# Kernel optimization log

Measured on AMD Instinct MI355X. Metric: run time of the kernel, lower is better.

The kernel has to match this reference:

```python
import jax, jax.numpy as jnp
import numpy as np
import math

CEN_W = 1.0
ANG_W = 1.0


def _radius(ndim):
    # Iterative version of the recursive Radius() from the source.
    if ndim < 1:
        raise ValueError('ndim >= 1 required')
    if ndim == 1:
        return 0.0
    r = 0.5
    for _ in range(3, ndim + 1):
        r = 0.5 / math.sqrt(1.0 - r * r)
    return r


def _costheta(ndim):
    return 2.0 * _radius(ndim - 1) ** 2 - 1.0


def setup_inputs() -> dict:
    key = jax.random.key(0)
    k1, k2, k3 = jax.random.split(key, 3)
    B, C, D = 65536, 1000, 512
    y = jax.random.randint(k1, (B,), 0, C, dtype=jnp.int64 if jax.config.jax_enable_x64 else jnp.int32)
    feat = jax.random.normal(k2, (B, D), dtype=jnp.float32)
    centers = jax.random.normal(k3, (C, D), dtype=jnp.float32)
    return {"y": y, "feat": feat, "centers": centers}


def reference(y, feat, centers):
    C = centers.shape[0]
    B = feat.shape[0]
    ct = jnp.float32(_costheta(C))  # static Python constant from num_classes

    # ---- center loss: gather assigned centers, squared diff sum ----
    centers_pred = centers[y]                      # [B, D] gather
    diff = feat - centers_pred
    loss_cen = 0.5 * jnp.sum(diff * diff) / B

    # ---- angular loss: vectorized Gram matrix over classes ----
    # In torch, centers[j].data and dist are detached -> stop_gradient here.
    centers_sg = jax.lax.stop_gradient(centers)
    dist = jnp.linalg.norm(centers_sg, axis=1)     # [C], detached
    gram = centers @ centers_sg.T                  # [C, C]; grad flows via rows only
    sim = gram / (dist[:, None] * dist[None, :])
    offdiag = 1.0 - jnp.eye(C, dtype=sim.dtype)
    loss_ang = jnp.sum(offdiag * (sim - ct) ** 2) / (0.5 * C * (C - 1))

    return loss_cen * CEN_W + loss_ang * ANG_W
```

## Files before the change

### kernel.cpp

```cpp
#include <hip/hip_runtime.h>
#include <math.h>

typedef __attribute__((ext_vector_type(8))) short bf16x8;
typedef __attribute__((ext_vector_type(16))) float f32x16;
typedef __attribute__((ext_vector_type(4))) float vf4;
typedef __attribute__((ext_vector_type(4))) unsigned int u32x4;

__device__ __forceinline__ float wave_reduce(float v) {
#pragma unroll
    for (int off = 32; off > 0; off >>= 1) v += __shfl_down(v, off, 64);
    return v;
}

__device__ __forceinline__ unsigned int pk_trunc(float f0, float f1) {
    unsigned u0 = __float_as_uint(f0), u1 = __float_as_uint(f1);
    return (u1 & 0xFFFF0000u) | (u0 >> 16);
}

__global__ __launch_bounds__(256) void fused_kernel(const int* __restrict__ y,
                                                    const vf4* __restrict__ feat4,
                                                    const vf4* __restrict__ cent4,
                                                    float* __restrict__ partials,
                                                    int n4, int d4, float cen_scale,
                                                    int C, int ntile32, int steps16,
                                                    float ct, float ang_scale) {
    const int bid = blockIdx.x;
    const int lane = threadIdx.x & 63;
    const int wid = threadIdx.x >> 6;
    __shared__ float sm[4];

    float partial = 0.f;

    const int t = bid * 4 + wid;
    const int ntile2 = ntile32 * ntile32;
    if (t < ntile2) {
        const int ti = t / ntile32;
        const int tj = t - ti * ntile32;
        const int m = lane & 31;
        const int half = lane >> 5;
        const int ra = ti * 32 + m;
        const int rb = tj * 32 + m;
        const bool va = ra < C;
        const bool vb = rb < C;
        const vf4* aptr = cent4 + (size_t)ra * d4 + half * 2;
        const vf4* bptr = cent4 + (size_t)rb * d4 + half * 2;
        f32x16 acc;
#pragma unroll
        for (int k = 0; k < 16; ++k) acc[k] = 0.f;
        float sa = 0.f, sb = 0.f;
#pragma unroll 4
        for (int st = 0; st < steps16; ++st) {
            vf4 a0 = {0.f, 0.f, 0.f, 0.f}, a1 = a0, b0 = a0, b1 = a0;
            if (va) { a0 = aptr[st * 4]; a1 = aptr[st * 4 + 1]; }
            if (vb) { b0 = bptr[st * 4]; b1 = bptr[st * 4 + 1]; }
            sa += a0.x * a0.x + a0.y * a0.y + a0.z * a0.z + a0.w * a0.w
                + a1.x * a1.x + a1.y * a1.y + a1.z * a1.z + a1.w * a1.w;
            sb += b0.x * b0.x + b0.y * b0.y + b0.z * b0.z + b0.w * b0.w
                + b1.x * b1.x + b1.y * b1.y + b1.z * b1.z + b1.w * b1.w;
            u32x4 ap, bp;
            ap.x = pk_trunc(a0.x, a0.y); ap.y = pk_trunc(a0.z, a0.w);
            ap.z = pk_trunc(a1.x, a1.y); ap.w = pk_trunc(a1.z, a1.w);
            bp.x = pk_trunc(b0.x, b0.y); bp.y = pk_trunc(b0.z, b0.w);
            bp.z = pk_trunc(b1.x, b1.y); bp.w = pk_trunc(b1.z, b1.w);
            bf16x8 af = __builtin_bit_cast(bf16x8, ap);
            bf16x8 bf = __builtin_bit_cast(bf16x8, bp);
            acc = __builtin_amdgcn_mfma_f32_32x32x16_bf16(af, bf, acc, 0, 0, 0);
        }
        sa += __shfl_xor(sa, 32, 64);
        sb += __shfl_xor(sb, 32, 64);
        const int gj = tj * 32 + m;
        const float dj = sb;
        float local = 0.f;
#pragma unroll
        for (int reg = 0; reg < 16; ++reg) {
            const int r = (reg & 3) + 8 * (reg >> 2) + 4 * half;
            const int gi = ti * 32 + r;
            const float di = __shfl(sa, r, 64);
            if (gi < C && gj < C && gi != gj) {
                float sim = acc[reg] * rsqrtf(di * dj);
                float dlt = sim - ct;
                local += dlt * dlt;
            }
        }
        partial = local * ang_scale;
    }

    {
        const int stride = gridDim.x * 256;
        float cs = 0.f;
        int i = bid * 256 + threadIdx.x;
        if ((stride % d4) == 0) {
            if (i < n4) {
                int row = i / d4;
                const int col = i - row * d4;
                const int rstep = stride / d4;
                for (; i < n4; i += stride, row += rstep) {
                    const int cls = y[row];
                    vf4 f = __builtin_nontemporal_load(feat4 + i);
                    vf4 c = cent4[(size_t)cls * d4 + col];
                    float dx = f.x - c.x, dy = f.y - c.y, dz = f.z - c.z, dw = f.w - c.w;
                    cs += dx * dx + dy * dy + dz * dz + dw * dw;
                }
            }
        } else {
            for (; i < n4; i += stride) {
                int row = i / d4;
                int col = i - row * d4;
                const int cls = y[row];
                vf4 f = __builtin_nontemporal_load(feat4 + i);
                vf4 c = cent4[(size_t)cls * d4 + col];
                float dx = f.x - c.x, dy = f.y - c.y, dz = f.z - c.z, dw = f.w - c.w;
                cs += dx * dx + dy * dy + dz * dz + dw * dw;
            }
        }
        partial += cs * cen_scale;
    }

    float r = wave_reduce(partial);
    if (lane == 0) sm[wid] = r;
    __syncthreads();
    if (threadIdx.x == 0) {
        partials[bid] = sm[0] + sm[1] + sm[2] + sm[3];
    }
}

__global__ __launch_bounds__(256) void reduce_kernel(const float* __restrict__ partials,
                                                     float* __restrict__ out, int nb) {
    __shared__ float sm[4];
    const int lane = threadIdx.x & 63;
    const int wid = threadIdx.x >> 6;
    float s = 0.f;
    for (int i = threadIdx.x; i < nb; i += 256) s += partials[i];
    s = wave_reduce(s);
    if (lane == 0) sm[wid] = s;
    __syncthreads();
    if (threadIdx.x == 0) out[0] = sm[0] + sm[1] + sm[2] + sm[3];
}

extern "C" void kernel_launch(void* const* d_in, const int* in_sizes, int n_in,
                              void* d_out, int out_size, void* d_ws, size_t ws_size,
                              hipStream_t stream) {
    const int* y = (const int*)d_in[0];
    const float* feat = (const float*)d_in[1];
    const float* centers = (const float*)d_in[2];

    const int B = in_sizes[0];
    const int D = in_sizes[1] / B;
    const int C = in_sizes[2] / D;
    const int d4 = D / 4;
    const int ntile32 = (C + 31) / 32;

    const int nd = C - 1;
    double r = 0.0;
    if (nd >= 2) {
        r = 0.5;
        for (int i = 3; i <= nd; ++i) r = 0.5 / sqrt(1.0 - r * r);
    }
    const float ct = (float)(2.0 * r * r - 1.0);

    const float cen_scale = (float)(0.5 / (double)B);
    const float ang_scale = (float)(1.0 / (0.5 * (double)C * (double)(C - 1)));

    float* partials = (float*)d_ws;
    const int nb = 8192;

    fused_kernel<<<nb, 256, 0, stream>>>(
        y, (const vf4*)feat, (const vf4*)centers, partials,
        B * d4, d4, cen_scale, C, ntile32, D / 16, ct, ang_scale);

    reduce_kernel<<<1, 256, 0, stream>>>(partials, (float*)d_out, nb);
}
```

Baseline: 210.6 us.

## Exploit Gram symmetry, unroll center-loss loads, fuse final reduction via atomic counter

The angular part now computes only the upper-triangular 32x32 tiles of the Gram matrix and weights off-diagonal tiles by two, roughly halving the MFMA work and center reloads. The center-loss loop is replaced, for the exact-fit shape, by four independent feature and gather loads per thread to expose memory-level parallelism. The separate reduce kernel is dropped in favour of a last-block-done reduction using an atomic counter, which is zeroed with a memset before launch. This saves a kernel launch but adds a memset and relies on the fast-path shape conditions and the threadfence ordering.

Result: slower. 569.0 us (+170.1%).

```diff
diff --git a/kernel.cpp b/kernel.cpp
--- a/kernel.cpp
+++ b/kernel.cpp
@@ -21,21 +21,33 @@
                                                     const vf4* __restrict__ feat4,
                                                     const vf4* __restrict__ cent4,
                                                     float* __restrict__ partials,
+                                                    unsigned int* __restrict__ counter,
+                                                    float* __restrict__ out,
                                                     int n4, int d4, float cen_scale,
-                                                    int C, int ntile32, int steps16,
-                                                    float ct, float ang_scale) {
+                                                    int C, int ntile32, int ntri,
+                                                    int steps16, float ct, float ang_scale) {
     const int bid = blockIdx.x;
     const int lane = threadIdx.x & 63;
     const int wid = threadIdx.x >> 6;
     __shared__ float sm[4];
+    __shared__ bool is_last;
 
     float partial = 0.f;
 
     const int t = bid * 4 + wid;
-    const int ntile2 = ntile32 * ntile32;
-    if (t < ntile2) {
-        const int ti = t / ntile32;
-        const int tj = t - ti * ntile32;
+    if (t < ntri) {
+        const int N = ntile32;
+        const float ff = (float)((2 * N + 1) * (2 * N + 1) - 8 * t);
+        int ti = (int)(((float)(2 * N + 1) - sqrtf(ff)) * 0.5f);
+        int base = ti * N - (ti * (ti - 1)) / 2;
+        if (t < base) {
+            --ti; base = ti * N - (ti * (ti - 1)) / 2;
+        } else {
+            const int nxt = (ti + 1) * N - ((ti + 1) * ti) / 2;
+            if (t >= nxt) { ++ti; base = nxt; }
+        }
+        const int tj = ti + (t - base);
+
         const int m = lane & 31;
         const int half = lane >> 5;
         const int ra = ti * 32 + m;
@@ -82,26 +94,41 @@
                 local += dlt * dlt;
             }
         }
-        partial = local * ang_scale;
+        const float w = (ti == tj) ? 1.f : 2.f;
+        partial = local * (ang_scale * w);
     }
 
     {
         const int stride = gridDim.x * 256;
         float cs = 0.f;
         int i = bid * 256 + threadIdx.x;
-        if ((stride % d4) == 0) {
-            if (i < n4) {
-                int row = i / d4;
-                const int col = i - row * d4;
-                const int rstep = stride / d4;
-                for (; i < n4; i += stride, row += rstep) {
-                    const int cls = y[row];
-                    vf4 f = __builtin_nontemporal_load(feat4 + i);
-                    vf4 c = cent4[(size_t)cls * d4 + col];
-                    float dx = f.x - c.x, dy = f.y - c.y, dz = f.z - c.z, dw = f.w - c.w;
-                    cs += dx * dx + dy * dy + dz * dz + dw * dw;
-                }
-            }
+        const bool fast = ((stride % d4) == 0) && ((d4 & 63) == 0) && (n4 == 4 * stride);
+        if (fast) {
+            int row = i / d4;
+            const int col = i - row * d4;
+            const int rstep = stride / d4;
+            const vf4 f0 = __builtin_nontemporal_load(feat4 + i);
+            const vf4 f1 = __builtin_nontemporal_load(feat4 + i + stride);
+            const vf4 f2 = __builtin_nontemporal_load(feat4 + i + 2 * stride);
+            const vf4 f3 = __builtin_nontemporal_load(feat4 + i + 3 * stride);
+            const int r0 = __builtin_amdgcn_readfirstlane(row);
+            const int cls0 = y[r0];
+            const int cls1 = y[r0 + rstep];
+            const int cls2 = y[r0 + 2 * rstep];
+            const int cls3 = y[r0 + 3 * rstep];
+            const vf4 g0 = cent4[(size_t)cls0 * d4 + col];
+            const vf4 g1 = cent4[(size_t)cls1 * d4 + col];
+            const vf4 g2 = cent4[(size_t)cls2 * d4 + col];
+            const vf4 g3 = cent4[(size_t)cls3 * d4 + col];
+            float dx, dy, dz, dw;
+            dx = f0.x - g0.x; dy = f0.y - g0.y; dz = f0.z - g0.z; dw = f0.w - g0.w;
+            cs += dx * dx + dy * dy + dz * dz + dw * dw;
+            dx = f1.x - g1.x; dy = f1.y - g1.y; dz = f1.z - g1.z; dw = f1.w - g1.w;
+            cs += dx * dx + dy * dy + dz * dz + dw * dw;
+            dx = f2.x - g2.x; dy = f2.y - g2.y; dz = f2.z - g2.z; dw = f2.w - g2.w;
+            cs += dx * dx + dy * dy + dz * dz + dw * dw;
+            dx = f3.x - g3.x; dy = f3.y - g3.y; dz = f3.z - g3.z; dw = f3.w - g3.w;
+            cs += dx * dx + dy * dy + dz * dz + dw * dw;
         } else {
             for (; i < n4; i += stride) {
                 int row = i / d4;
@@ -121,20 +148,21 @@
     __syncthreads();
     if (threadIdx.x == 0) {
         partials[bid] = sm[0] + sm[1] + sm[2] + sm[3];
-    }
-}
-
-__global__ __launch_bounds__(256) void reduce_kernel(const float* __restrict__ partials,
-                                                     float* __restrict__ out, int nb) {
-    __shared__ float sm[4];
-    const int lane = threadIdx.x & 63;
-    const int wid = threadIdx.x >> 6;
-    float s = 0.f;
-    for (int i = threadIdx.x; i < nb; i += 256) s += partials[i];
-    s = wave_reduce(s);
-    if (lane == 0) sm[wid] = s;
+        __threadfence();
+        const unsigned int old = atomicAdd(counter, 1u);
+        is_last = (old == gridDim.x - 1);
+    }
     __syncthreads();
-    if (threadIdx.x == 0) out[0] = sm[0] + sm[1] + sm[2] + sm[3];
+    if (is_last) {
+        __threadfence();
+        float s = 0.f;
+        const int nbk = (int)gridDim.x;
+        for (int j = threadIdx.x; j < nbk; j += 256) s += partials[j];
+        s = wave_reduce(s);
+        if (lane == 0) sm[wid] = s;
+        __syncthreads();
+        if (threadIdx.x == 0) out[0] = sm[0] + sm[1] + sm[2] + sm[3];
+    }
 }
 
 extern "C" void kernel_launch(void* const* d_in, const int* in_sizes, int n_in,
@@ -149,6 +177,7 @@
     const int C = in_sizes[2] / D;
     const int d4 = D / 4;
     const int ntile32 = (C + 31) / 32;
+    const int ntri = ntile32 * (ntile32 + 1) / 2;
 
     const int nd = C - 1;
     double r = 0.0;
@@ -161,12 +190,12 @@
     const float cen_scale = (float)(0.5 / (double)B);
     const float ang_scale = (float)(1.0 / (0.5 * (double)C * (double)(C - 1)));
 
-    float* partials = (float*)d_ws;
+    unsigned int* counter = (unsigned int*)d_ws;
+    float* partials = (float*)d_ws + 64;
     const int nb = 8192;
 
+    hipMemsetAsync(d_ws, 0, 4, stream);
     fused_kernel<<<nb, 256, 0, stream>>>(
-        y, (const vf4*)feat, (const vf4*)centers, partials,
-        B * d4, d4, cen_scale, C, ntile32, D / 16, ct, ang_scale);
-
-    reduce_kernel<<<1, 256, 0, stream>>>(partials, (float*)d_out, nb);
-}
+        y, (const vf4*)feat, (const vf4*)centers, partials, counter, (float*)d_out,
+        B * d4, d4, cen_scale, C, ntile32, ntri, D / 16, ct, ang_scale);
+}
```
